# Kernel optimization log

Hardware: AMD Instinct MI355X
Metric: run time of the kernel (lower is better)

Reference implementation:

```python
import jax, jax.numpy as jnp
import numpy as np


def setup_inputs() -> dict:
    key = jax.random.key(0)
    k1, k2, k3, k4 = jax.random.split(key, 4)
    B, S, D_IN, D_OUT, R = 4, 2048, 4096, 4096, 8
    x = jax.random.normal(k1, (B, S, D_IN), dtype=jnp.float32)
    hra_u = jax.random.normal(k2, (D_IN, R), dtype=jnp.float32)
    base_weight = jax.random.normal(k3, (D_OUT, D_IN), dtype=jnp.float32) * 0.02
    bias = jax.random.normal(k4, (D_OUT,), dtype=jnp.float32) * 0.02
    return {"x": x, "hra_u": hra_u, "base_weight": base_weight, "bias": bias}


def reference(x, hra_u, base_weight, bias):
    # HRALinear forward (not merged, apply_GS=False):
    #   u_i = hra_u[:, i] / ||hra_u[:, i]||
    #   delta = (I - 2 u_0 u_0^T) @ ... @ (I - 2 u_{r-1} u_{r-1}^T)
    #   out = x @ (base_weight @ delta)^T + bias
    # Equivalent rank-1 form: W <- W - 2 (W u_i) u_i^T, sequentially over i.
    u = hra_u / jnp.linalg.norm(hra_u, axis=0, keepdims=True)  # [D_in, r]

    def step(W, ui):
        # W: [D_out, D_in], ui: [D_in]
        Wu = W @ ui                       # [D_out]
        return W - 2.0 * Wu[:, None] * ui[None, :], None

    new_weight, _ = jax.lax.scan(step, base_weight, u.T)  # scan over r columns
    out = jnp.einsum("bsd,od->bso", x, new_weight) + bias
    return out
```

## Files before the change

kernel.cpp:

```cpp
#include <hip/hip_runtime.h>
#include <stdint.h>

#define DIN 4096
#define DOUT 4096
#define RNK 8
#define MROWS 8192

typedef unsigned short u16;
typedef __attribute__((ext_vector_type(8))) short short8;
typedef __attribute__((ext_vector_type(8))) unsigned short u16x8;
typedef __attribute__((ext_vector_type(4))) float f32x4;

__device__ __forceinline__ u16 f2bf(float f) {
    union { float f; uint32_t u; } v; v.f = f;
    uint32_t u = v.u;
    uint32_t r = (u + 0x7fffu + ((u >> 16) & 1u)) >> 16;
    return (u16)r;
}

__device__ __forceinline__ void gl_lds16(const u16* g, u16* lds) {
    __builtin_amdgcn_global_load_lds((const __attribute__((address_space(1))) unsigned int*)g,
                                     (__attribute__((address_space(3))) unsigned int*)lds,
                                     16, 0, 0);
}

__global__ __launch_bounds__(256) void k_normalize_u(const float* __restrict__ hra_u,
                                                     float* __restrict__ Un) {
    const int i = blockIdx.x;
    const int t = threadIdx.x;
    float ss = 0.f;
    for (int d = t; d < DIN; d += 256) {
        float v = hra_u[d * RNK + i];
        ss += v * v;
    }
    for (int off = 32; off; off >>= 1) ss += __shfl_down(ss, off, 64);
    __shared__ float red[4];
    if ((t & 63) == 0) red[t >> 6] = ss;
    __syncthreads();
    float inv = rsqrtf(red[0] + red[1] + red[2] + red[3]);
    for (int d = t; d < DIN; d += 256)
        Un[i * DIN + d] = hra_u[d * RNK + i] * inv;
}

__global__ __launch_bounds__(256) void k_gram(const float* __restrict__ Un,
                                              float* __restrict__ G) {
    const int t = threadIdx.x;
    float acc[RNK][RNK] = {};
    for (int d = t; d < DIN; d += 256) {
        float u[RNK];
        #pragma unroll
        for (int i = 0; i < RNK; i++) u[i] = Un[i * DIN + d];
        #pragma unroll
        for (int i = 0; i < RNK; i++)
            #pragma unroll
            for (int j = 0; j < RNK; j++)
                acc[i][j] += u[i] * u[j];
    }
    #pragma unroll
    for (int i = 0; i < RNK; i++)
        #pragma unroll
        for (int j = 0; j < RNK; j++)
            for (int off = 32; off; off >>= 1)
                acc[i][j] += __shfl_down(acc[i][j], off, 64);
    __shared__ float red[4][64];
    if ((t & 63) == 0) {
        #pragma unroll
        for (int i = 0; i < RNK; i++)
            #pragma unroll
            for (int j = 0; j < RNK; j++)
                red[t >> 6][i * RNK + j] = acc[i][j];
    }
    __syncthreads();
    if (t < 64) G[t] = red[0][t] + red[1][t] + red[2][t] + red[3][t];
}

__global__ __launch_bounds__(256) void k_wy_build(const float* __restrict__ W,
                                                  const float* __restrict__ Un,
                                                  const float* __restrict__ G,
                                                  u16* __restrict__ Wb) {
    const int o = blockIdx.x;
    const int t = threadIdx.x;
    const float* wrow = W + (size_t)o * DIN;

    float4 wv[4];
    float acc[RNK] = {};
    #pragma unroll
    for (int j = 0; j < 4; j++) {
        const int c = t + j * 256;
        wv[j] = *(const float4*)(wrow + c * 4);
        #pragma unroll
        for (int i = 0; i < RNK; i++) {
            float4 uv = *(const float4*)(Un + i * DIN + c * 4);
            acc[i] += wv[j].x * uv.x + wv[j].y * uv.y + wv[j].z * uv.z + wv[j].w * uv.w;
        }
    }
    #pragma unroll
    for (int i = 0; i < RNK; i++)
        for (int off = 32; off; off >>= 1)
            acc[i] += __shfl_down(acc[i], off, 64);
    __shared__ float red[4][RNK];
    __shared__ float ysh[RNK];
    if ((t & 63) == 0) {
        #pragma unroll
        for (int i = 0; i < RNK; i++) red[t >> 6][i] = acc[i];
    }
    __syncthreads();
    if (t == 0) {
        float y[RNK];
        #pragma unroll
        for (int i = 0; i < RNK; i++) {
            float s = red[0][i] + red[1][i] + red[2][i] + red[3][i];
            for (int j = 0; j < i; j++) s -= y[j] * G[j * RNK + i];
            y[i] = 2.f * s;
            ysh[i] = y[i];
        }
    }
    __syncthreads();
    float y[RNK];
    #pragma unroll
    for (int i = 0; i < RNK; i++) y[i] = ysh[i];

    #pragma unroll
    for (int j = 0; j < 4; j++) {
        const int c = t + j * 256;
        float4 r = wv[j];
        #pragma unroll
        for (int i = 0; i < RNK; i++) {
            float4 uv = *(const float4*)(Un + i * DIN + c * 4);
            r.x -= y[i] * uv.x; r.y -= y[i] * uv.y;
            r.z -= y[i] * uv.z; r.w -= y[i] * uv.w;
        }
        ushort4 ov;
        ov.x = f2bf(r.x); ov.y = f2bf(r.y); ov.z = f2bf(r.z); ov.w = f2bf(r.w);
        *(ushort4*)(Wb + (size_t)o * DIN + c * 4) = ov;
    }
}

__global__ __launch_bounds__(256) void k_cast_x(const float* __restrict__ x,
                                                u16* __restrict__ xb) {
    const size_t total = (size_t)MROWS * DIN / 8;
    for (size_t idx = (size_t)blockIdx.x * 256 + threadIdx.x; idx < total;
         idx += (size_t)2048 * 256) {
        float4 a = *(const float4*)(x + idx * 8);
        float4 b = *(const float4*)(x + idx * 8 + 4);
        u16x8 o;
        o[0] = f2bf(a.x); o[1] = f2bf(a.y); o[2] = f2bf(a.z); o[3] = f2bf(a.w);
        o[4] = f2bf(b.x); o[5] = f2bf(b.y); o[6] = f2bf(b.z); o[7] = f2bf(b.w);
        *(u16x8*)(xb + idx * 8) = o;
    }
}

__global__ __launch_bounds__(512, 2) void k_gemm(const u16* __restrict__ A,
                                                 const u16* __restrict__ B,
                                                 const float* __restrict__ bias,
                                                 float* __restrict__ C) {
    __shared__ u16 sm[65536];

    const int t = threadIdx.x;
    const int w = t >> 6, l = t & 63;
    const int bm = blockIdx.x & 31;
    const int bn = blockIdx.x >> 5;
    const int wm = w >> 2, wn = w & 3;

    const int quad = l >> 4, lane16 = l & 15;

    const int lc   = (l & 7) ^ (l >> 3);
    const int prow = lc >> 2;
    const int kch  = lc & 3;
    const int rA0  = (2 * w) * 16 + 2 * (l >> 3) + prow;
    const u16* agp0 = A + (size_t)(bm * 256 + rA0) * DIN + kch * 8;
    const u16* agp1 = agp0 + (size_t)16 * DIN;
    const u16* bgp0 = B + (size_t)(bn * 256 + rA0) * DIN + kch * 8;
    const u16* bgp1 = bgp0 + (size_t)16 * DIN;
    const int ldso0 = (2 * w) * 512;
    const int ldso1 = (2 * w + 1) * 512;

    const int pA    = (((lane16 & 1) * 4 + quad) ^ ((lane16 >> 1) & 7)) * 8;
    const int a_off = (wm * 64 + (lane16 >> 1)) * 64 + pA;
    const int b_off = (wn * 32 + (lane16 >> 1)) * 64 + pA;

    f32x4 acc[8][4] = {};

    const int NT = DIN / 32;

    #pragma unroll
    for (int tt = 0; tt < 3; tt++) {
        u16* Asw = sm + tt * 16384;
        u16* Bsw = Asw + 8192;
        const int kc = tt * 32;
        gl_lds16(agp0 + kc, Asw + ldso0);
        gl_lds16(agp1 + kc, Asw + ldso1);
        gl_lds16(bgp0 + kc, Bsw + ldso0);
        gl_lds16(bgp1 + kc, Bsw + ldso1);
    }
    asm volatile("s_waitcnt vmcnt(8)" ::: "memory");
    __builtin_amdgcn_s_barrier();

    for (int kt = 0; kt < NT; kt++) {
        const u16* Asb = sm + (kt & 3) * 16384;
        const u16* Bsb = Asb + 8192;
        const bool pf = (kt + 3) < NT;
        u16* As3 = sm + ((kt + 3) & 3) * 16384;
        u16* Bs3 = As3 + 8192;
        const int kc3 = (kt + 3) * 32;

        short8 a0[4], bfr[4];
        #pragma unroll
        for (int mt = 0; mt < 4; mt++)
            a0[mt] = *(const short8*)&Asb[a_off + (mt * 8) * 64];
        #pragma unroll
        for (int nt = 0; nt < 4; nt++)
            bfr[nt] = *(const short8*)&Bsb[b_off + (nt * 8) * 64];
        if (pf) {
            gl_lds16(agp0 + kc3, As3 + ldso0);
            gl_lds16(agp1 + kc3, As3 + ldso1);
        }
        __builtin_amdgcn_s_barrier();
        asm volatile("s_waitcnt lgkmcnt(0)" ::: "memory");
        __builtin_amdgcn_s_setprio(1);
        #pragma unroll
        for (int mt = 0; mt < 4; mt++)
            #pragma unroll
            for (int nt = 0; nt < 4; nt++)
                acc[mt][nt] = __builtin_amdgcn_mfma_f32_16x16x32_bf16(
                    a0[mt], bfr[nt], acc[mt][nt], 0, 0, 0);
        __builtin_amdgcn_s_setprio(0);
        __builtin_amdgcn_s_barrier();

        short8 a1[4];
        #pragma unroll
        for (int mt = 0; mt < 4; mt++)
            a1[mt] = *(const short8*)&Asb[a_off + (32 + mt * 8) * 64];
        if (pf) {
            gl_lds16(bgp0 + kc3, Bs3 + ldso0);
            gl_lds16(bgp1 + kc3, Bs3 + ldso1);
        }
        __builtin_amdgcn_s_barrier();
        asm volatile("s_waitcnt lgkmcnt(0)" ::: "memory");
        __builtin_amdgcn_s_setprio(1);
        #pragma unroll
        for (int mt = 0; mt < 4; mt++)
            #pragma unroll
            for (int nt = 0; nt < 4; nt++)
                acc[4 + mt][nt] = __builtin_amdgcn_mfma_f32_16x16x32_bf16(
                    a1[mt], bfr[nt], acc[4 + mt][nt], 0, 0, 0);
        __builtin_amdgcn_s_setprio(0);
        asm volatile("s_waitcnt vmcnt(8)" ::: "memory");
        __builtin_amdgcn_s_barrier();
    }

    const int col0 = bn * 256 + wn * 64 + lane16;
    const int row00 = bm * 256 + wm * 128 + quad * 4;
    float bv[4];
    #pragma unroll
    for (int nt = 0; nt < 4; nt++) bv[nt] = bias[col0 + nt * 16];
    #pragma unroll
    for (int half = 0; half < 2; half++) {
        #pragma unroll
        for (int mt = 0; mt < 4; mt++) {
            const int row0 = row00 + half * 64 + mt * 16;
            #pragma unroll
            for (int nt = 0; nt < 4; nt++) {
                #pragma unroll
                for (int rr = 0; rr < 4; rr++) {
                    C[(size_t)(row0 + rr) * DOUT + col0 + nt * 16] =
                        acc[half * 4 + mt][nt][rr] + bv[nt];
                }
            }
        }
    }
}

extern "C" void kernel_launch(void* const* d_in, const int* in_sizes, int n_in,
                              void* d_out, int out_size, void* d_ws, size_t ws_size,
                              hipStream_t stream) {
    const float* x     = (const float*)d_in[0];
    const float* hra_u = (const float*)d_in[1];
    const float* W     = (const float*)d_in[2];
    const float* bias  = (const float*)d_in[3];
    float* out = (float*)d_out;

    char* ws = (char*)d_ws;
    float* Un = (float*)(ws);
    float* G  = (float*)(ws + 131072);
    u16*   Wb = (u16*)(ws + 524288);
    u16*   xb = (u16*)(ws + 524288 + 33554432);

    k_normalize_u<<<RNK, 256, 0, stream>>>(hra_u, Un);
    k_gram<<<1, 256, 0, stream>>>(Un, G);
    k_wy_build<<<DOUT, 256, 0, stream>>>(W, Un, G, Wb);
    k_cast_x<<<2048, 256, 0, stream>>>(x, xb);
    k_gemm<<<(MROWS / 256) * (DOUT / 256), 512, 0, stream>>>(xb, Wb, bias, out);
}
```

Baseline: 562.8 us.

## Fuse normalize and Gram prep, stage U in LDS, software-pipeline GEMM fragment loads

Merges the normalization and Gram kernels into one k_prep kernel that computes the Gram matrix from raw hra_u and rescales it, removing a launch. The WY build now stages all normalized U vectors in LDS (128KB) and processes 16 rows per block, one wave per row pair, so U is not re-read from global memory for every row. The GEMM main loop is unrolled by two with ping-pong B fragment registers, and the next tile's fragments are loaded before the second MFMA half, which overlaps LDS reads with compute. Prefetch is made unconditional with wrapped addresses, so some redundant loads occur at the tail. The large LDS allocation limits WY-build occupancy.

Measured after the change: 627.2 us. 11.4% more time.

```diff
diff --git a/kernel.cpp b/kernel.cpp
--- a/kernel.cpp
+++ b/kernel.cpp
@@ -5,6 +5,7 @@
 #define DOUT 4096
 #define RNK 8
 #define MROWS 8192
+#define NTILES 128
 
 typedef unsigned short u16;
 typedef __attribute__((ext_vector_type(8))) short short8;
@@ -24,115 +25,120 @@
                                      16, 0, 0);
 }
 
-__global__ __launch_bounds__(256) void k_normalize_u(const float* __restrict__ hra_u,
-                                                     float* __restrict__ Un) {
-    const int i = blockIdx.x;
+__global__ __launch_bounds__(1024) void k_prep(const float* __restrict__ hra_u,
+                                               float* __restrict__ Un,
+                                               float* __restrict__ G) {
     const int t = threadIdx.x;
-    float ss = 0.f;
-    for (int d = t; d < DIN; d += 256) {
-        float v = hra_u[d * RNK + i];
-        ss += v * v;
-    }
-    for (int off = 32; off; off >>= 1) ss += __shfl_down(ss, off, 64);
-    __shared__ float red[4];
-    if ((t & 63) == 0) red[t >> 6] = ss;
+    float s[64];
+    #pragma unroll
+    for (int k = 0; k < 64; k++) s[k] = 0.f;
+    for (int d = t; d < DIN; d += 1024) {
+        float4 p = *(const float4*)(hra_u + d * 8);
+        float4 q = *(const float4*)(hra_u + d * 8 + 4);
+        float v[8] = {p.x, p.y, p.z, p.w, q.x, q.y, q.z, q.w};
+        #pragma unroll
+        for (int i = 0; i < 8; i++)
+            #pragma unroll
+            for (int j = 0; j < 8; j++)
+                s[i * 8 + j] += v[i] * v[j];
+    }
+    #pragma unroll
+    for (int k = 0; k < 64; k++)
+        for (int off = 32; off; off >>= 1)
+            s[k] += __shfl_down(s[k], off, 64);
+    __shared__ float red[16][64];
+    __shared__ float Sg[64];
+    __shared__ float inv[8];
+    if ((t & 63) == 0) {
+        #pragma unroll
+        for (int k = 0; k < 64; k++) red[t >> 6][k] = s[k];
+    }
     __syncthreads();
-    float inv = rsqrtf(red[0] + red[1] + red[2] + red[3]);
-    for (int d = t; d < DIN; d += 256)
-        Un[i * DIN + d] = hra_u[d * RNK + i] * inv;
-}
-
-__global__ __launch_bounds__(256) void k_gram(const float* __restrict__ Un,
-                                              float* __restrict__ G) {
-    const int t = threadIdx.x;
-    float acc[RNK][RNK] = {};
-    for (int d = t; d < DIN; d += 256) {
-        float u[RNK];
-        #pragma unroll
-        for (int i = 0; i < RNK; i++) u[i] = Un[i * DIN + d];
-        #pragma unroll
-        for (int i = 0; i < RNK; i++)
-            #pragma unroll
-            for (int j = 0; j < RNK; j++)
-                acc[i][j] += u[i] * u[j];
-    }
-    #pragma unroll
-    for (int i = 0; i < RNK; i++)
-        #pragma unroll
-        for (int j = 0; j < RNK; j++)
-            for (int off = 32; off; off >>= 1)
-                acc[i][j] += __shfl_down(acc[i][j], off, 64);
-    __shared__ float red[4][64];
-    if ((t & 63) == 0) {
-        #pragma unroll
-        for (int i = 0; i < RNK; i++)
-            #pragma unroll
-            for (int j = 0; j < RNK; j++)
-                red[t >> 6][i * RNK + j] = acc[i][j];
+    if (t < 64) {
+        float tot = 0.f;
+        #pragma unroll
+        for (int w = 0; w < 16; w++) tot += red[w][t];
+        Sg[t] = tot;
     }
     __syncthreads();
-    if (t < 64) G[t] = red[0][t] + red[1][t] + red[2][t] + red[3][t];
-}
-
-__global__ __launch_bounds__(256) void k_wy_build(const float* __restrict__ W,
+    if (t < 8) inv[t] = rsqrtf(Sg[t * 8 + t]);
+    __syncthreads();
+    if (t < 64) G[t] = Sg[t] * inv[t >> 3] * inv[t & 7];
+    float iv[8];
+    #pragma unroll
+    for (int i = 0; i < 8; i++) iv[i] = inv[i];
+    for (int d = t; d < DIN; d += 1024) {
+        float4 p = *(const float4*)(hra_u + d * 8);
+        float4 q = *(const float4*)(hra_u + d * 8 + 4);
+        Un[0 * DIN + d] = p.x * iv[0];
+        Un[1 * DIN + d] = p.y * iv[1];
+        Un[2 * DIN + d] = p.z * iv[2];
+        Un[3 * DIN + d] = p.w * iv[3];
+        Un[4 * DIN + d] = q.x * iv[4];
+        Un[5 * DIN + d] = q.y * iv[5];
+        Un[6 * DIN + d] = q.z * iv[6];
+        Un[7 * DIN + d] = q.w * iv[7];
+    }
+}
+
+__global__ __launch_bounds__(512) void k_wy_build(const float* __restrict__ W,
                                                   const float* __restrict__ Un,
                                                   const float* __restrict__ G,
                                                   u16* __restrict__ Wb) {
-    const int o = blockIdx.x;
+    __shared__ float Us[RNK * DIN];
     const int t = threadIdx.x;
-    const float* wrow = W + (size_t)o * DIN;
-
-    float4 wv[4];
-    float acc[RNK] = {};
-    #pragma unroll
-    for (int j = 0; j < 4; j++) {
-        const int c = t + j * 256;
-        wv[j] = *(const float4*)(wrow + c * 4);
-        #pragma unroll
-        for (int i = 0; i < RNK; i++) {
-            float4 uv = *(const float4*)(Un + i * DIN + c * 4);
-            acc[i] += wv[j].x * uv.x + wv[j].y * uv.y + wv[j].z * uv.z + wv[j].w * uv.w;
+    #pragma unroll
+    for (int j = 0; j < 16; j++) {
+        const int c = t + 512 * j;
+        *(float4*)&Us[c * 4] = *(const float4*)&Un[c * 4];
+    }
+    __syncthreads();
+    const int wv = t >> 6, l = t & 63;
+    #pragma unroll 1
+    for (int rr = 0; rr < 2; rr++) {
+        const int row = blockIdx.x * 16 + wv * 2 + rr;
+        const float* wrow = W + (size_t)row * DIN;
+        float4 wc[16];
+        float acc[RNK] = {};
+        #pragma unroll
+        for (int j = 0; j < 16; j++) {
+            const int c = l + 64 * j;
+            wc[j] = *(const float4*)(wrow + c * 4);
+            #pragma unroll
+            for (int i = 0; i < RNK; i++) {
+                float4 uv = *(const float4*)&Us[(i * 1024 + c) * 4];
+                acc[i] += wc[j].x * uv.x + wc[j].y * uv.y + wc[j].z * uv.z + wc[j].w * uv.w;
+            }
         }
-    }
-    #pragma unroll
-    for (int i = 0; i < RNK; i++)
-        for (int off = 32; off; off >>= 1)
-            acc[i] += __shfl_down(acc[i], off, 64);
-    __shared__ float red[4][RNK];
-    __shared__ float ysh[RNK];
-    if ((t & 63) == 0) {
-        #pragma unroll
-        for (int i = 0; i < RNK; i++) red[t >> 6][i] = acc[i];
-    }
-    __syncthreads();
-    if (t == 0) {
-        float y[RNK];
-        #pragma unroll
-        for (int i = 0; i < RNK; i++) {
-            float s = red[0][i] + red[1][i] + red[2][i] + red[3][i];
-            for (int j = 0; j < i; j++) s -= y[j] * G[j * RNK + i];
-            y[i] = 2.f * s;
-            ysh[i] = y[i];
+        #pragma unroll
+        for (int i = 0; i < RNK; i++)
+            for (int off = 32; off; off >>= 1)
+                acc[i] += __shfl_down(acc[i], off, 64);
+        float yv[RNK];
+        if (l == 0) {
+            #pragma unroll
+            for (int i = 0; i < RNK; i++) {
+                float s2 = acc[i];
+                for (int j = 0; j < i; j++) s2 -= yv[j] * G[j * RNK + i];
+                yv[i] = 2.f * s2;
+            }
         }
-    }
-    __syncthreads();
-    float y[RNK];
-    #pragma unroll
-    for (int i = 0; i < RNK; i++) y[i] = ysh[i];
-
-    #pragma unroll
-    for (int j = 0; j < 4; j++) {
-        const int c = t + j * 256;
-        float4 r = wv[j];
-        #pragma unroll
-        for (int i = 0; i < RNK; i++) {
-            float4 uv = *(const float4*)(Un + i * DIN + c * 4);
-            r.x -= y[i] * uv.x; r.y -= y[i] * uv.y;
-            r.z -= y[i] * uv.z; r.w -= y[i] * uv.w;
+        #pragma unroll
+        for (int i = 0; i < RNK; i++) yv[i] = __shfl(yv[i], 0, 64);
+        #pragma unroll
+        for (int j = 0; j < 16; j++) {
+            const int c = l + 64 * j;
+            float4 r = wc[j];
+            #pragma unroll
+            for (int i = 0; i < RNK; i++) {
+                float4 uv = *(const float4*)&Us[(i * 1024 + c) * 4];
+                r.x -= yv[i] * uv.x; r.y -= yv[i] * uv.y;
+                r.z -= yv[i] * uv.z; r.w -= yv[i] * uv.w;
+            }
+            ushort4 ov;
+            ov.x = f2bf(r.x); ov.y = f2bf(r.y); ov.z = f2bf(r.z); ov.w = f2bf(r.w);
+            *(ushort4*)(Wb + (size_t)row * DIN + c * 4) = ov;
         }
-        ushort4 ov;
-        ov.x = f2bf(r.x); ov.y = f2bf(r.y); ov.z = f2bf(r.z); ov.w = f2bf(r.w);
-        *(ushort4*)(Wb + (size_t)o * DIN + c * 4) = ov;
     }
 }
 
@@ -180,74 +186,78 @@
     const int b_off = (wn * 32 + (lane16 >> 1)) * 64 + pA;
 
     f32x4 acc[8][4] = {};
-
-    const int NT = DIN / 32;
+    short8 a0[4], a1[4], bA[4], bB[4];
 
     #pragma unroll
     for (int tt = 0; tt < 3; tt++) {
         u16* Asw = sm + tt * 16384;
-        u16* Bsw = Asw + 8192;
         const int kc = tt * 32;
         gl_lds16(agp0 + kc, Asw + ldso0);
         gl_lds16(agp1 + kc, Asw + ldso1);
-        gl_lds16(bgp0 + kc, Bsw + ldso0);
-        gl_lds16(bgp1 + kc, Bsw + ldso1);
+        gl_lds16(bgp0 + kc, Asw + 8192 + ldso0);
+        gl_lds16(bgp1 + kc, Asw + 8192 + ldso1);
     }
     asm volatile("s_waitcnt vmcnt(8)" ::: "memory");
     __builtin_amdgcn_s_barrier();
-
-    for (int kt = 0; kt < NT; kt++) {
-        const u16* Asb = sm + (kt & 3) * 16384;
-        const u16* Bsb = Asb + 8192;
-        const bool pf = (kt + 3) < NT;
-        u16* As3 = sm + ((kt + 3) & 3) * 16384;
-        u16* Bs3 = As3 + 8192;
-        const int kc3 = (kt + 3) * 32;
-
-        short8 a0[4], bfr[4];
-        #pragma unroll
-        for (int mt = 0; mt < 4; mt++)
-            a0[mt] = *(const short8*)&Asb[a_off + (mt * 8) * 64];
-        #pragma unroll
-        for (int nt = 0; nt < 4; nt++)
-            bfr[nt] = *(const short8*)&Bsb[b_off + (nt * 8) * 64];
-        if (pf) {
-            gl_lds16(agp0 + kc3, As3 + ldso0);
-            gl_lds16(agp1 + kc3, As3 + ldso1);
-        }
-        __builtin_amdgcn_s_barrier();
-        asm volatile("s_waitcnt lgkmcnt(0)" ::: "memory");
-        __builtin_amdgcn_s_setprio(1);
-        #pragma unroll
-        for (int mt = 0; mt < 4; mt++)
-            #pragma unroll
-            for (int nt = 0; nt < 4; nt++)
-                acc[mt][nt] = __builtin_amdgcn_mfma_f32_16x16x32_bf16(
-                    a0[mt], bfr[nt], acc[mt][nt], 0, 0, 0);
-        __builtin_amdgcn_s_setprio(0);
-        __builtin_amdgcn_s_barrier();
-
-        short8 a1[4];
-        #pragma unroll
-        for (int mt = 0; mt < 4; mt++)
-            a1[mt] = *(const short8*)&Asb[a_off + (32 + mt * 8) * 64];
-        if (pf) {
-            gl_lds16(bgp0 + kc3, Bs3 + ldso0);
-            gl_lds16(bgp1 + kc3, Bs3 + ldso1);
-        }
-        __builtin_amdgcn_s_barrier();
-        asm volatile("s_waitcnt lgkmcnt(0)" ::: "memory");
-        __builtin_amdgcn_s_setprio(1);
-        #pragma unroll
-        for (int mt = 0; mt < 4; mt++)
-            #pragma unroll
-            for (int nt = 0; nt < 4; nt++)
-                acc[4 + mt][nt] = __builtin_amdgcn_mfma_f32_16x16x32_bf16(
-                    a1[mt], bfr[nt], acc[4 + mt][nt], 0, 0, 0);
-        __builtin_amdgcn_s_setprio(0);
-        asm volatile("s_waitcnt vmcnt(8)" ::: "memory");
-        __builtin_amdgcn_s_barrier();
-    }
+    #pragma unroll
+    for (int mt = 0; mt < 4; mt++) a0[mt] = *(const short8*)&sm[a_off + (mt * 8) * 64];
+    #pragma unroll
+    for (int nt = 0; nt < 4; nt++) bA[nt] = *(const short8*)&sm[8192 + b_off + (nt * 8) * 64];
+
+#define TILE_BODY(KT, BC, BN)                                                         \
+    {                                                                                 \
+        u16* As_c = sm + ((KT) & 3) * 16384;                                          \
+        u16* As_n = sm + (((KT) + 1) & 3) * 16384;                                    \
+        u16* As_s = sm + (((KT) + 3) & 3) * 16384;                                    \
+        const int kc3 = (((KT) + 3) & (NTILES - 1)) * 32;                             \
+                                     \
+        _Pragma("unroll")                                                             \
+        for (int mt = 0; mt < 4; mt++)                                                \
+            a1[mt] = *(const short8*)&As_c[a_off + (32 + mt * 8) * 64];               \
+        gl_lds16(agp0 + kc3, As_s + ldso0);                                           \
+        gl_lds16(agp1 + kc3, As_s + ldso1);                                           \
+        __builtin_amdgcn_sched_barrier(0);                                            \
+        __builtin_amdgcn_s_barrier();                                                 \
+                                                                              \
+        __builtin_amdgcn_s_setprio(1);                                                \
+        _Pragma("unroll")                                                             \
+        for (int mt = 0; mt < 4; mt++)                                                \
+            _Pragma("unroll")                                                         \
+            for (int nt = 0; nt < 4; nt++)                                            \
+                acc[mt][nt] = __builtin_amdgcn_mfma_f32_16x16x32_bf16(                \
+                    a0[mt], BC[nt], acc[mt][nt], 0, 0, 0);                            \
+        __builtin_amdgcn_s_setprio(0);                                                \
+        asm volatile("s_waitcnt vmcnt(6)" ::: "memory");                              \
+        __builtin_amdgcn_s_barrier();                                                 \
+                                         \
+        _Pragma("unroll")                                                             \
+        for (int mt = 0; mt < 4; mt++)                                                \
+            a0[mt] = *(const short8*)&As_n[a_off + (mt * 8) * 64];                    \
+        _Pragma("unroll")                                                             \
+        for (int nt = 0; nt < 4; nt++)                                                \
+            BN[nt] = *(const short8*)&As_n[8192 + b_off + (nt * 8) * 64];             \
+        gl_lds16(bgp0 + kc3, As_s + 8192 + ldso0);                                    \
+        gl_lds16(bgp1 + kc3, As_s + 8192 + ldso1);                                    \
+        __builtin_amdgcn_sched_barrier(0);                                            \
+        __builtin_amdgcn_s_barrier();                                                 \
+                                                                              \
+        __builtin_amdgcn_s_setprio(1);                                                \
+        _Pragma("unroll")                                                             \
+        for (int mt = 0; mt < 4; mt++)                                                \
+            _Pragma("unroll")                                                         \
+            for (int nt = 0; nt < 4; nt++)                                            \
+                acc[4 + mt][nt] = __builtin_amdgcn_mfma_f32_16x16x32_bf16(            \
+                    a1[mt], BC[nt], acc[4 + mt][nt], 0, 0, 0);                        \
+        __builtin_amdgcn_s_setprio(0);                                                \
+        __builtin_amdgcn_s_barrier();                                                 \
+    }
+
+    #pragma unroll 1
+    for (int kt2 = 0; kt2 < NTILES; kt2 += 2) {
+        TILE_BODY(kt2,     bA, bB)
+        TILE_BODY(kt2 + 1, bB, bA)
+    }
+#undef TILE_BODY
 
     const int col0 = bn * 256 + wn * 64 + lane16;
     const int row00 = bm * 256 + wm * 128 + quad * 4;
@@ -286,9 +296,8 @@
     u16*   Wb = (u16*)(ws + 524288);
     u16*   xb = (u16*)(ws + 524288 + 33554432);
 
-    k_normalize_u<<<RNK, 256, 0, stream>>>(hra_u, Un);
-    k_gram<<<1, 256, 0, stream>>>(Un, G);
-    k_wy_build<<<DOUT, 256, 0, stream>>>(W, Un, G, Wb);
+    k_prep<<<1, 1024, 0, stream>>>(hra_u, Un, G);
+    k_wy_build<<<DOUT / 16, 512, 0, stream>>>(W, Un, G, Wb);
     k_cast_x<<<2048, 256, 0, stream>>>(x, xb);
     k_gemm<<<(MROWS / 256) * (DOUT / 256), 512, 0, stream>>>(xb, Wb, bias, out);
 }
```
